# Performance work log

Hardware: AMD Instinct MI355X
Metric: run time of the kernel (lower is better)

Reference implementation:

```python
import jax, jax.numpy as jnp
import numpy as np

NUM_CLASSES = 1000
NEG_SLOPE = 0.01  # torch F.leaky_relu default


def setup_inputs() -> dict:
    key = jax.random.key(0)
    k1, k2, k3, k4 = jax.random.split(key, 4)
    B, D, M = 64, 768, 2048
    input_embeddings = jax.random.normal(k1, (B, D), dtype=jnp.float32)
    memory_embeddings = jax.random.normal(k2, (B, D, M), dtype=jnp.float32)
    memory_labels = jax.random.randint(k3, (B, M), 0, NUM_CLASSES, dtype=jnp.int64)
    # orthogonal-ish init is irrelevant for numerics testing; use gaussian params
    kq, kk = jax.random.split(k4)
    W_Q = jax.random.normal(kq, (D, D), dtype=jnp.float32) / jnp.sqrt(jnp.float32(D))
    W_K = jax.random.normal(kk, (D, D), dtype=jnp.float32) / jnp.sqrt(jnp.float32(D))
    return {
        "input_embeddings": input_embeddings,
        "memory_embeddings": memory_embeddings,
        "memory_labels": memory_labels,
        "W_Q": W_Q,
        "W_K": W_K,
    }


def reference(input_embeddings, memory_embeddings, memory_labels, W_Q, W_K):
    # q = x @ W_K : [B, D]
    q = input_embeddings @ W_K
    # k = W_Q @ memory_tensor (broadcast over batch) : [B, D, M]
    # scores = leaky_relu(q . k) : [B, M]
    scores = jnp.einsum("bd,de,bem->bm", input_embeddings, W_K @ W_Q, memory_embeddings)
    scores = jnp.where(scores >= 0, scores, NEG_SLOPE * scores)
    # combine with one-hot labels == scatter-add scores into class bins : [B, C]
    def scatter_row(s, lab):
        return jnp.zeros((NUM_CLASSES,), dtype=s.dtype).at[lab].add(s)
    logits = jax.vmap(scatter_row)(scores, memory_labels)
    return jax.nn.softmax(logits, axis=1)
```

## Files before the change

### kernel.cpp

```cpp
#include <hip/hip_runtime.h>

#define BB 64
#define DD 768
#define MM 2048
#define CC 1000
#define NEG 0.01f
#define ECH 8
#define EPER (DD / ECH)

__global__ __launch_bounds__(256) void gemm64(const float* __restrict__ A,
                                              const float* __restrict__ W,
                                              float* __restrict__ out) {
    __shared__ float as[DD];
    const int r = blockIdx.x;
    const int c = blockIdx.y * 256 + threadIdx.x;
    for (int k = threadIdx.x; k < DD; k += 256) as[k] = A[r * DD + k];
    __syncthreads();
    float acc = 0.f;
#pragma unroll 8
    for (int k = 0; k < DD; ++k) acc = fmaf(as[k], W[k * DD + c], acc);
    out[r * DD + c] = acc;
}

__global__ __launch_bounds__(512) void scores_partial(const float* __restrict__ mem,
                                                      const float* __restrict__ q2,
                                                      float* __restrict__ part) {
    const int b = blockIdx.x;
    const int ec = blockIdx.y;
    const int e0 = ec * EPER;
    __shared__ float qs[EPER];
    if (threadIdx.x < EPER) qs[threadIdx.x] = q2[b * DD + e0 + threadIdx.x];
    __syncthreads();

    const float4* mp = (const float4*)(mem + ((size_t)b * DD + e0) * MM);
    const int m4 = threadIdx.x;
    float4 acc = {0.f, 0.f, 0.f, 0.f};
#pragma unroll 4
    for (int e = 0; e < EPER; ++e) {
        const float q = qs[e];
        const float4 v = mp[(size_t)e * (MM / 4) + m4];
        acc.x = fmaf(q, v.x, acc.x);
        acc.y = fmaf(q, v.y, acc.y);
        acc.z = fmaf(q, v.z, acc.z);
        acc.w = fmaf(q, v.w, acc.w);
    }
    ((float4*)(part + ((size_t)b * ECH + ec) * MM))[m4] = acc;
}

__global__ __launch_bounds__(256) void finalize(const float* __restrict__ part,
                                                const int* __restrict__ labels,
                                                float* __restrict__ out) {
    __shared__ float logits[CC];
    __shared__ float red[16];
    const int b = blockIdx.x;

    for (int i = threadIdx.x; i < CC; i += 256) logits[i] = 0.f;
    __syncthreads();

    for (int m = threadIdx.x; m < MM; m += 256) {
        float s = 0.f;
#pragma unroll
        for (int ec = 0; ec < ECH; ++ec)
            s += part[((size_t)b * ECH + ec) * MM + m];
        s = (s >= 0.f) ? s : NEG * s;
        const int lab = labels[b * MM + m];
        atomicAdd(&logits[lab], s);
    }
    __syncthreads();

    float mx = -INFINITY;
    for (int i = threadIdx.x; i < CC; i += 256) mx = fmaxf(mx, logits[i]);
#pragma unroll
    for (int o = 1; o < 64; o <<= 1) mx = fmaxf(mx, __shfl_xor(mx, o, 64));
    const int wid = threadIdx.x >> 6;
    if ((threadIdx.x & 63) == 0) red[wid] = mx;
    __syncthreads();
    mx = fmaxf(fmaxf(red[0], red[1]), fmaxf(red[2], red[3]));

    float sm = 0.f;
    for (int i = threadIdx.x; i < CC; i += 256) sm += expf(logits[i] - mx);
#pragma unroll
    for (int o = 1; o < 64; o <<= 1) sm += __shfl_xor(sm, o, 64);
    if ((threadIdx.x & 63) == 0) red[8 + wid] = sm;
    __syncthreads();
    sm = red[8] + red[9] + red[10] + red[11];

    const float inv = 1.f / sm;
    for (int i = threadIdx.x; i < CC; i += 256)
        out[b * CC + i] = expf(logits[i] - mx) * inv;
}

extern "C" void kernel_launch(void* const* d_in, const int* in_sizes, int n_in,
                              void* d_out, int out_size, void* d_ws, size_t ws_size,
                              hipStream_t stream) {
    const float* x      = (const float*)d_in[0];
    const float* mem    = (const float*)d_in[1];
    const int*   labels = (const int*)d_in[2];
    const float* W_Q    = (const float*)d_in[3];
    const float* W_K    = (const float*)d_in[4];
    float* out = (float*)d_out;

    float* ws   = (float*)d_ws;
    float* q1   = ws;
    float* q2   = ws + BB * DD;
    float* part = ws + 2 * BB * DD;

    gemm64<<<dim3(BB, DD / 256), 256, 0, stream>>>(x, W_K, q1);
    gemm64<<<dim3(BB, DD / 256), 256, 0, stream>>>(q1, W_Q, q2);
    scores_partial<<<dim3(BB, ECH), 512, 0, stream>>>(mem, q2, part);
    finalize<<<BB, 256, 0, stream>>>(part, labels, out);
}
```

Before: 646.2 us.

## Fuse score dot product with label scatter and restructure GEMMs and softmax

```diff
diff --git a/kernel.cpp b/kernel.cpp
--- a/kernel.cpp
+++ b/kernel.cpp
@@ -5,89 +5,89 @@
 #define MM 2048
 #define CC 1000
 #define NEG 0.01f
-#define ECH 8
-#define EPER (DD / ECH)
 
-__global__ __launch_bounds__(256) void gemm64(const float* __restrict__ A,
-                                              const float* __restrict__ W,
-                                              float* __restrict__ out) {
-    __shared__ float as[DD];
-    const int r = blockIdx.x;
-    const int c = blockIdx.y * 256 + threadIdx.x;
-    for (int k = threadIdx.x; k < DD; k += 256) as[k] = A[r * DD + k];
-    __syncthreads();
-    float acc = 0.f;
+__global__ __launch_bounds__(512) void rowgemm_k(const float* __restrict__ A,
+                                                 const float* __restrict__ W,
+                                                 float* __restrict__ out,
+                                                 float* __restrict__ zero_buf,
+                                                 int zero_n) {
+    const int gt = blockIdx.x * 512 + threadIdx.x;
+    const int r = gt / DD;
+    const int c = gt - r * DD;
+    const float* a = A + r * DD;
+    const float* w = W + c;
+    float acc0 = 0.f, acc1 = 0.f;
 #pragma unroll 8
-    for (int k = 0; k < DD; ++k) acc = fmaf(as[k], W[k * DD + c], acc);
-    out[r * DD + c] = acc;
+    for (int d = 0; d < DD; d += 2) {
+        acc0 = fmaf(a[d], w[(size_t)d * DD], acc0);
+        acc1 = fmaf(a[d + 1], w[(size_t)(d + 1) * DD], acc1);
+    }
+    out[gt] = acc0 + acc1;
+    if (zero_buf != nullptr) {
+        for (int i = gt; i < zero_n; i += 96 * 512) zero_buf[i] = 0.f;
+    }
 }
 
-__global__ __launch_bounds__(512) void scores_partial(const float* __restrict__ mem,
-                                                      const float* __restrict__ q2,
-                                                      float* __restrict__ part) {
+__global__ __launch_bounds__(512) void scores_scatter_k(const float* __restrict__ mem,
+                                                        const float* __restrict__ q2,
+                                                        const int* __restrict__ labels,
+                                                        float* __restrict__ logits_g) {
     const int b = blockIdx.x;
-    const int ec = blockIdx.y;
-    const int e0 = ec * EPER;
-    __shared__ float qs[EPER];
-    if (threadIdx.x < EPER) qs[threadIdx.x] = q2[b * DD + e0 + threadIdx.x];
+    const int m = blockIdx.y * 512 + threadIdx.x;
+    __shared__ float qs[DD];
+    __shared__ float lg[CC];
+    for (int i = threadIdx.x; i < DD; i += 512) qs[i] = q2[b * DD + i];
+    for (int i = threadIdx.x; i < CC; i += 512) lg[i] = 0.f;
     __syncthreads();
 
-    const float4* mp = (const float4*)(mem + ((size_t)b * DD + e0) * MM);
-    const int m4 = threadIdx.x;
-    float4 acc = {0.f, 0.f, 0.f, 0.f};
-#pragma unroll 4
-    for (int e = 0; e < EPER; ++e) {
-        const float q = qs[e];
-        const float4 v = mp[(size_t)e * (MM / 4) + m4];
-        acc.x = fmaf(q, v.x, acc.x);
-        acc.y = fmaf(q, v.y, acc.y);
-        acc.z = fmaf(q, v.z, acc.z);
-        acc.w = fmaf(q, v.w, acc.w);
-    }
-    ((float4*)(part + ((size_t)b * ECH + ec) * MM))[m4] = acc;
+    const float* mp = mem + (size_t)b * DD * MM + m;
+    float acc = 0.f;
+#pragma unroll 16
+    for (int e = 0; e < DD; ++e)
+        acc = fmaf(qs[e], mp[(size_t)e * MM], acc);
+
+    acc = (acc >= 0.f) ? acc : NEG * acc;
+    atomicAdd(&lg[labels[b * MM + m]], acc);
+    __syncthreads();
+
+    for (int i = threadIdx.x; i < CC; i += 512)
+        if (lg[i] != 0.f) atomicAdd(&logits_g[b * CC + i], lg[i]);
 }
 
-__global__ __launch_bounds__(256) void finalize(const float* __restrict__ part,
-                                                const int* __restrict__ labels,
-                                                float* __restrict__ out) {
-    __shared__ float logits[CC];
-    __shared__ float red[16];
+__global__ __launch_bounds__(256) void softmax_k(const float* __restrict__ lg,
+                                                 float* __restrict__ out) {
     const int b = blockIdx.x;
+    const int tid = threadIdx.x;
+    __shared__ float red[8];
+    const int base = b * CC;
 
-    for (int i = threadIdx.x; i < CC; i += 256) logits[i] = 0.f;
-    __syncthreads();
+    float v0 = lg[base + tid];
+    float v1 = lg[base + tid + 256];
+    float v2 = lg[base + tid + 512];
+    float v3 = (tid < CC - 768) ? lg[base + tid + 768] : -INFINITY;
 
-    for (int m = threadIdx.x; m < MM; m += 256) {
-        float s = 0.f;
-#pragma unroll
-        for (int ec = 0; ec < ECH; ++ec)
-            s += part[((size_t)b * ECH + ec) * MM + m];
-        s = (s >= 0.f) ? s : NEG * s;
-        const int lab = labels[b * MM + m];
-        atomicAdd(&logits[lab], s);
-    }
-    __syncthreads();
-
-    float mx = -INFINITY;
-    for (int i = threadIdx.x; i < CC; i += 256) mx = fmaxf(mx, logits[i]);
+    float mx = fmaxf(fmaxf(v0, v1), fmaxf(v2, v3));
 #pragma unroll
     for (int o = 1; o < 64; o <<= 1) mx = fmaxf(mx, __shfl_xor(mx, o, 64));
-    const int wid = threadIdx.x >> 6;
-    if ((threadIdx.x & 63) == 0) red[wid] = mx;
+    if ((tid & 63) == 0) red[tid >> 6] = mx;
     __syncthreads();
     mx = fmaxf(fmaxf(red[0], red[1]), fmaxf(red[2], red[3]));
 
-    float sm = 0.f;
-    for (int i = threadIdx.x; i < CC; i += 256) sm += expf(logits[i] - mx);
+    v0 = expf(v0 - mx);
+    v1 = expf(v1 - mx);
+    v2 = expf(v2 - mx);
+    v3 = (tid < CC - 768) ? expf(v3 - mx) : 0.f;
+    float sm = v0 + v1 + v2 + v3;
 #pragma unroll
     for (int o = 1; o < 64; o <<= 1) sm += __shfl_xor(sm, o, 64);
-    if ((threadIdx.x & 63) == 0) red[8 + wid] = sm;
+    if ((tid & 63) == 0) red[4 + (tid >> 6)] = sm;
     __syncthreads();
-    sm = red[8] + red[9] + red[10] + red[11];
+    const float inv = 1.f / (red[4] + red[5] + red[6] + red[7]);
 
-    const float inv = 1.f / sm;
-    for (int i = threadIdx.x; i < CC; i += 256)
-        out[b * CC + i] = expf(logits[i] - mx) * inv;
+    out[base + tid] = v0 * inv;
+    out[base + tid + 256] = v1 * inv;
+    out[base + tid + 512] = v2 * inv;
+    if (tid < CC - 768) out[base + tid + 768] = v3 * inv;
 }
 
 extern "C" void kernel_launch(void* const* d_in, const int* in_sizes, int n_in,
@@ -100,13 +100,13 @@
     const float* W_K    = (const float*)d_in[4];
     float* out = (float*)d_out;
 
-    float* ws   = (float*)d_ws;
-    float* q1   = ws;
-    float* q2   = ws + BB * DD;
-    float* part = ws + 2 * BB * DD;
+    float* ws       = (float*)d_ws;
+    float* q1       = ws;
+    float* q2       = ws + BB * DD;
+    float* logits_g = ws + 2 * BB * DD;
 
-    gemm64<<<dim3(BB, DD / 256), 256, 0, stream>>>(x, W_K, q1);
-    gemm64<<<dim3(BB, DD / 256), 256, 0, stream>>>(q1, W_Q, q2);
-    scores_partial<<<dim3(BB, ECH), 512, 0, stream>>>(mem, q2, part);
-    finalize<<<BB, 256, 0, stream>>>(part, labels, out);
+    rowgemm_k<<<96, 512, 0, stream>>>(x, W_K, q1, nullptr, 0);
+    rowgemm_k<<<96, 512, 0, stream>>>(q1, W_Q, q2, logits_g, BB * CC);
+    scores_scatter_k<<<dim3(BB, MM / 512), 512, 0, stream>>>(mem, q2, labels, logits_g);
+    softmax_k<<<BB, 256, 0, stream>>>(logits_g, out);
 }
```

New measurement: 617.7 us. 1.05x faster.
